# Kernel optimization log

Hardware: AMD Instinct MI355X
Metric: run time of the kernel (lower is better)

Reference implementation:

```python
import jax, jax.numpy as jnp
from jax import lax
import numpy as np

# --- constants from Vessel_Enhance_Block defaults ---
MIN_MAX = (0.0, 500.0)
ALPHA, BETA, GAMMA = 0.5, 1.0, 5.0          # frangi_param[0:3]
SIGMAS = tuple(np.arange(1.0, 2.5, 0.3).tolist())  # [1.0,1.3,1.6,1.9,2.2]
FRANGI_TH = 0.2
TH_LO, TH_HI = 0.1, 0.5                     # th_param
MIN_SIZE = 200


def _gauss_kernel1d(sigma, order):
    """scipy.ndimage-style Gaussian derivative kernel (truncate=4)."""
    radius = int(4.0 * sigma + 0.5)
    x = np.arange(-radius, radius + 1)
    phi = np.exp(-0.5 * x ** 2 / sigma ** 2)
    phi /= phi.sum()
    if order == 0:
        return phi
    exps = np.arange(order + 1)
    q = np.zeros(order + 1); q[0] = 1.0
    D = np.diag(exps[1:], 1)
    P = np.diag(np.full(order, -1.0 / sigma ** 2), -1)
    for _ in range(order):
        q = (D + P) @ q
    return (x[:, None].astype(float) ** exps @ q) * phi


def _corr1d(x, k, axis):
    """scipy gaussian_filter1d == correlate with k[::-1] == convolve with k.
    lax.conv is a correlation, so pass k reversed. mode='reflect' (symmetric)."""
    x = jnp.moveaxis(x, axis, -1)
    shp = x.shape
    r = (k.shape[0] - 1) // 2
    xp = jnp.pad(x.reshape(-1, 1, shp[-1]), ((0, 0), (0, 0), (r, r)), mode='symmetric')
    kern = jnp.asarray(k[::-1].copy(), x.dtype).reshape(1, 1, -1)
    y = lax.conv_general_dilated(xp, kern, (1,), 'VALID')
    return jnp.moveaxis(y.reshape(shp), -1, axis)


def _frangi(img):
    """2D Frangi vesselness, black_ridges=False, img: [B,H,W]."""
    img = -img  # black_ridges=False -> negate image
    out = jnp.zeros_like(img)
    for sigma in SIGMAS:
        k0 = _gauss_kernel1d(sigma, 0)
        k1 = _gauss_kernel1d(sigma, 1)
        k2 = _gauss_kernel1d(sigma, 2)
        s2 = jnp.asarray(sigma ** 2, img.dtype)  # scale normalization
        Hrr = _corr1d(_corr1d(img, k2, 1), k0, 2) * s2
        Hrc = _corr1d(_corr1d(img, k1, 1), k1, 2) * s2
        Hcc = _corr1d(_corr1d(img, k0, 1), k2, 2) * s2
        mid = 0.5 * (Hrr + Hcc)
        disc = jnp.sqrt(jnp.square(0.5 * (Hrr - Hcc)) + jnp.square(Hrc))
        e_hi, e_lo = mid + disc, mid - disc
        small = jnp.abs(e_hi) <= jnp.abs(e_lo)  # sort eigenvalues by magnitude
        lam1 = jnp.where(small, e_hi, e_lo)     # |lam1| <= |lam2|
        lam2 = jnp.where(small, e_lo, e_hi)
        lam2c = jnp.maximum(lam2, 1e-10)
        r_b2 = jnp.square(lam1 / lam2c)                       # blobness^2
        s_sq = jnp.square(lam1) + jnp.square(lam2)            # structuredness^2
        vals = jnp.exp(-r_b2 / (2.0 * BETA ** 2)) * (1.0 - jnp.exp(-s_sq / (2.0 * GAMMA ** 2)))
        out = jnp.maximum(out, vals)
    return out


def _remove_small(mask, min_size):
    """remove_small_objects(connectivity=2): drop 8-connected components < min_size."""
    H, W = mask.shape
    BIG = H * W
    idx = jnp.arange(BIG, dtype=jnp.int32).reshape(H, W)
    lab0 = jnp.where(mask, idx, BIG)

    def nmin(lab):  # min over 8-neighborhood, restricted to mask
        p = jnp.pad(lab, 1, constant_values=BIG)
        m = lab
        for di in (0, 1, 2):
            for dj in (0, 1, 2):
                if di == 1 and dj == 1:
                    continue
                m = jnp.minimum(m, lax.dynamic_slice(p, (di, dj), (H, W)))
        return jnp.where(mask, m, BIG)

    def jump(lab):  # pointer jumping: lab <- lab[lab]
        flat = lab.reshape(-1)
        ext = jnp.concatenate([flat, jnp.array([BIG], flat.dtype)])
        return ext[flat].reshape(H, W)

    def body(st):
        lab, _ = st
        return jump(jump(nmin(lab))), lab

    def cond(st):
        lab, prev = st
        return jnp.any(lab != prev)

    lab, _ = lax.while_loop(cond, body, (nmin(lab0), lab0))
    sizes = jnp.zeros(BIG + 1, jnp.int32).at[lab.reshape(-1)].add(mask.reshape(-1).astype(jnp.int32))
    return (sizes[lab] >= min_size) & mask


def setup_inputs() -> dict:
    key = jax.random.key(0)
    image = jax.random.uniform(key, (16, 1, 512, 512), dtype=jnp.float32)
    return {"image": image}


def reference(image):
    x = image[:, 0]                                   # [B,H,W]
    th_mask = (x >= TH_LO) & (x <= TH_HI)             # get_th
    scaled = x * (MIN_MAX[1] - MIN_MAX[0]) + MIN_MAX[0]
    fr = _frangi(scaled)
    fmask = th_mask & (fr >= FRANGI_TH)               # th & frangi masks
    out = jax.vmap(lambda m: _remove_small(m, MIN_SIZE))(fmask)
    return out[:, None]                               # [B,1,H,W] bool
```

## Files before the change

kernel.cpp:

```cpp
#include <hip/hip_runtime.h>
#include <math.h>
#include <string.h>

#define IMG_H   512
#define IMG_W   512
#define NPIX    (IMG_H*IMG_W)
#define NIMG    16
#define NSIG    5
#define MIN_SZ  200
#define SSTR    60
#define SROWS   52
#define TSTR    68
#define KVL     20
#define KHL     24
#define NBLK    65536

typedef float f4 __attribute__((ext_vector_type(4)));
typedef float f2 __attribute__((ext_vector_type(2)));

struct KTab {
  float kv[NSIG][3][KVL];
  float kh[NSIG][3][KHL];
  float s2[NSIG];
};

__device__ __forceinline__ void pkfma(f2 &acc, f2 x, f2 w) {
  asm("v_pk_fma_f32 %0, %1, %2, %0"
      : "+v"(acc) : "v"(x), "v"(w));
}

template<int SIG, int RAD, int MLO, int GH, int LP4, int L4P>
__device__ __forceinline__ void do_sigma(const float* __restrict__ sIn,
                                         float* __restrict__ t0,
                                         float* __restrict__ t1,
                                         float* __restrict__ t2,
                                         const KTab& kt, int tid, float* fr)
{
  if (tid < 32*GH) {
    int r0 = tid & 31;
    int h  = tid >> 5;
    int a  = (r0 + 9 - RAD)*SSTR + 4*(MLO + 2*h);
    f2 A0l={0,0},A0h={0,0},A1l={0,0},A1h={0,0},A2l={0,0},A2h={0,0};
    f2 B0l={0,0},B0h={0,0},B1l={0,0},B1h={0,0},B2l={0,0},B2h={0,0};
#pragma unroll 1
    for (int jj = 0; jj < LP4/4; ++jj) {
      f4 w0 = *(const f4*)&kt.kv[SIG][0][4*jj];
      f4 w1 = *(const f4*)&kt.kv[SIG][1][4*jj];
      f4 w2 = *(const f4*)&kt.kv[SIG][2][4*jj];
#pragma unroll
      for (int u = 0; u < 4; ++u) {
        f4 xA = *(const f4*)(sIn + a);
        f4 xB = *(const f4*)(sIn + a + 4);
        a += SSTR;
        f2 xAl = __builtin_shufflevector(xA, xA, 0, 1);
        f2 xAh = __builtin_shufflevector(xA, xA, 2, 3);
        f2 xBl = __builtin_shufflevector(xB, xB, 0, 1);
        f2 xBh = __builtin_shufflevector(xB, xB, 2, 3);
        f2 wv0 = {w0[u], w0[u]};
        f2 wv1 = {w1[u], w1[u]};
        f2 wv2 = {w2[u], w2[u]};
        pkfma(A0l, xAl, wv0); pkfma(A0h, xAh, wv0);
        pkfma(A1l, xAl, wv1); pkfma(A1h, xAh, wv1);
        pkfma(A2l, xAl, wv2); pkfma(A2h, xAh, wv2);
        pkfma(B0l, xBl, wv0); pkfma(B0h, xBh, wv0);
        pkfma(B1l, xBl, wv1); pkfma(B1h, xBh, wv1);
        pkfma(B2l, xBl, wv2); pkfma(B2h, xBh, wv2);
      }
    }
    int tb = r0*TSTR + 4*(MLO + 2*h);
    *(f4*)(t0 + tb)     = __builtin_shufflevector(A0l, A0h, 0,1,2,3);
    *(f4*)(t1 + tb)     = __builtin_shufflevector(A1l, A1h, 0,1,2,3);
    *(f4*)(t2 + tb)     = __builtin_shufflevector(A2l, A2h, 0,1,2,3);
    *(f4*)(t0 + tb + 4) = __builtin_shufflevector(B0l, B0h, 0,1,2,3);
    *(f4*)(t1 + tb + 4) = __builtin_shufflevector(B1l, B1h, 0,1,2,3);
    *(f4*)(t2 + tb + 4) = __builtin_shufflevector(B2l, B2h, 0,1,2,3);
  }
  __syncthreads();

  {
    int r  = tid >> 3;
    int c0 = (tid & 7) * 4;
    int wa = r*TSTR + 4*MLO + c0;
    f4 P0 = *(const f4*)(t0 + wa);
    f4 P1 = *(const f4*)(t1 + wa);
    f4 P2 = *(const f4*)(t2 + wa);
    f4 Q0 = *(const f4*)(t0 + wa + 4);
    f4 Q1 = *(const f4*)(t1 + wa + 4);
    f4 Q2 = *(const f4*)(t2 + wa + 4);
    wa += 8;
    f4 hrr={0,0,0,0}, hrc={0,0,0,0}, hcc={0,0,0,0};
#pragma unroll 1
    for (int aa = 0; aa < L4P/8; ++aa) {
      {
        f4 w0 = *(const f4*)&kt.kh[SIG][0][8*aa];
        f4 w1 = *(const f4*)&kt.kh[SIG][1][8*aa];
        f4 w2 = *(const f4*)&kt.kh[SIG][2][8*aa];
#pragma unroll
        for (int b = 0; b < 4; ++b)
#pragma unroll
          for (int k = 0; k < 4; ++k) {
            int e = b + k;
            float x2 = (e < 4) ? P2[e] : Q2[e-4];
            float x1 = (e < 4) ? P1[e] : Q1[e-4];
            float x0 = (e < 4) ? P0[e] : Q0[e-4];
            hrr[k] += x2 * w0[b];
            hrc[k] += x1 * w1[b];
            hcc[k] += x0 * w2[b];
          }
        P0 = *(const f4*)(t0 + wa);
        P1 = *(const f4*)(t1 + wa);
        P2 = *(const f4*)(t2 + wa);
      }
      {
        f4 w0 = *(const f4*)&kt.kh[SIG][0][8*aa+4];
        f4 w1 = *(const f4*)&kt.kh[SIG][1][8*aa+4];
        f4 w2 = *(const f4*)&kt.kh[SIG][2][8*aa+4];
#pragma unroll
        for (int b = 0; b < 4; ++b)
#pragma unroll
          for (int k = 0; k < 4; ++k) {
            int e = b + k;
            float x2 = (e < 4) ? Q2[e] : P2[e-4];
            float x1 = (e < 4) ? Q1[e] : P1[e-4];
            float x0 = (e < 4) ? Q0[e] : P0[e-4];
            hrr[k] += x2 * w0[b];
            hrc[k] += x1 * w1[b];
            hcc[k] += x0 * w2[b];
          }
        Q0 = *(const f4*)(t0 + wa + 4);
        Q1 = *(const f4*)(t1 + wa + 4);
        Q2 = *(const f4*)(t2 + wa + 4);
      }
      wa += 8;
    }
    float s2v = kt.s2[SIG];
#pragma unroll
    for (int k = 0; k < 4; ++k) {
      float Hrr = hrr[k]*s2v, Hrc = hrc[k]*s2v, Hcc = hcc[k]*s2v;
      float mid  = 0.5f*(Hrr + Hcc);
      float dif  = 0.5f*(Hrr - Hcc);
      float disc = sqrtf(dif*dif + Hrc*Hrc);
      float ehi  = mid + disc;
      float elo  = mid - disc;
      bool  sm   = fabsf(ehi) <= fabsf(elo);
      float lam1 = sm ? ehi : elo;
      float lam2 = sm ? elo : ehi;
      float lam2c = fmaxf(lam2, 1e-10f);
      float q    = lam1 / lam2c;
      float rb2  = q*q;
      float ssq  = lam1*lam1 + lam2*lam2;
      float v    = expf((-rb2)/2.0f) * (1.0f - expf((-ssq)/50.0f));
      fr[k] = fmaxf(fr[k], v);
    }
  }
  __syncthreads();
}

__global__ __launch_bounds__(256)
void frangi_label_kernel(const float* __restrict__ img,
                         int* __restrict__ labels,
                         int* __restrict__ parent,
                         int* __restrict__ bsizes,
                         KTab kt)
{
  __shared__ float sIn[SROWS*SSTR];
  __shared__ float t0[32*TSTR];
  __shared__ float t1[32*TSTR];
  __shared__ float t2[32*TSTR];

  const int tid    = threadIdx.x;
  const int imgIdx = blockIdx.y;
  const int tIdx   = blockIdx.x;
  const int tr0    = (tIdx >> 4) * 32;
  const int tc0    = (tIdx & 15) * 32;
  const float* __restrict__ im = img + (size_t)imgIdx * NPIX;

  for (int idx = tid; idx < SROWS*64; idx += 256) {
    int r  = idx >> 6;
    int cs = idx & 63;
    if (cs < SSTR) {
      float v = 0.0f;
      if (r < 50 && cs >= 3 && cs < 53) {
        int gr = tr0 + r - 9;
        int gc = tc0 + cs - 12;
        gr = (gr < 0) ? (-1 - gr) : ((gr >= IMG_H) ? (2*IMG_H - 1 - gr) : gr);
        gc = (gc < 0) ? (-1 - gc) : ((gc >= IMG_W) ? (2*IMG_W - 1 - gc) : gc);
        v = -(im[gr*IMG_W + gc] * 500.0f);
      }
      sIn[r*SSTR + cs] = v;
    }
  }
  __syncthreads();

  float fr[4] = {0.0f, 0.0f, 0.0f, 0.0f};
  do_sigma<0,  4,  2,  6, 12, 16>(sIn, t0, t1, t2, kt, tid, fr);
  do_sigma<1,  5,  1,  6, 12, 16>(sIn, t0, t1, t2, kt, tid, fr);
  do_sigma<2,  6,  1,  6, 16, 16>(sIn, t0, t1, t2, kt, tid, fr);
  do_sigma<3,  8,  1,  7, 20, 24>(sIn, t0, t1, t2, kt, tid, fr);
  do_sigma<4,  9,  0,  7, 20, 24>(sIn, t0, t1, t2, kt, tid, fr);

  const int r  = tid >> 3;
  const int c0 = (tid & 7) * 4;
  const int gr = tr0 + r;
  const size_t imgBase = (size_t)imgIdx * NPIX;
#pragma unroll
  for (int k = 0; k < 4; ++k) {
    int p = gr*IMG_W + tc0 + c0 + k;
    float x = im[p];
    bool m = (x >= 0.1f) && (x <= 0.5f) && (fr[k] >= 0.2f);
    labels[imgBase + p] = m ? p : -1;
  }
  {
    int blk = (tr0/2 + (tid >> 4))*256 + (tc0/2 + (tid & 15));
    int o   = (imgIdx << 16) + blk;
    parent[o] = blk;
    bsizes[o] = 0;
  }
}

__device__ __forceinline__ int ldA(const int* p) {
  return __hip_atomic_load(p, __ATOMIC_RELAXED, __HIP_MEMORY_SCOPE_AGENT);
}
__device__ __forceinline__ int rootOf(const int* L, int x) {
  int pa = ldA(&L[x]);
  while (pa != x) { int g = ldA(&L[pa]); x = pa; pa = g; }
  return x;
}
__device__ __forceinline__ void unite(int* P, int a, int b) {
  while (true) {
    a = rootOf(P, a);
    b = rootOf(P, b);
    if (a == b) return;
    int hi = a > b ? a : b;
    int lo = a ^ b ^ hi;
    int old = atomicCAS(&P[hi], hi, lo);
    if (old == hi) return;
    a = old; b = lo;
  }
}

__global__ __launch_bounds__(256)
void merge_kernel(const int* __restrict__ labels, int* __restrict__ parent)
{
  int gid = blockIdx.x*256 + threadIdx.x;
  int img = gid >> 16;
  int blk = gid & (NBLK - 1);
  int BR = blk >> 8, BC = blk & 255;
  const int* L = labels + ((size_t)img << 18);
  int p = BR*1024 + BC*2;
  int2 t = *(const int2*)(L + p);
  int2 bm = *(const int2*)(L + p + 512);
  bool f00 = t.x >= 0, f01 = t.y >= 0, f10 = bm.x >= 0, f11 = bm.y >= 0;
  if (!(f00 | f01 | f10 | f11)) return;
  int* P = parent + (img << 16);
  if (BC > 0 && (f00 | f10) && (L[p-1] >= 0 || L[p+511] >= 0))
    unite(P, blk, blk-1);
  if (BR > 0) {
    int2 n = *(const int2*)(L + p - 512);
    if ((f00 | f01) && (n.x >= 0 || n.y >= 0)) unite(P, blk, blk-256);
    if (BC > 0   && f00 && L[p-513] >= 0)      unite(P, blk, blk-257);
    if (BC < 255 && f01 && L[p-510] >= 0)      unite(P, blk, blk-255);
  }
}

__global__ __launch_bounds__(256)
void compress_count_kernel(const int* __restrict__ labels,
                           int* __restrict__ parent, int* __restrict__ bsizes)
{
  int gid = blockIdx.x*256 + threadIdx.x;
  int img = gid >> 16;
  int blk = gid & (NBLK - 1);
  int BR = blk >> 8, BC = blk & 255;
  const int* L = labels + ((size_t)img << 18);
  int p = BR*1024 + BC*2;
  int2 t = *(const int2*)(L + p);
  int2 bm = *(const int2*)(L + p + 512);
  int cnt = (t.x >= 0) + (t.y >= 0) + (bm.x >= 0) + (bm.y >= 0);
  int* P = parent + (img << 16);
  int rt = -1;
  if (cnt) {
    rt = rootOf(P, blk);
    __hip_atomic_store(&P[blk], rt, __ATOMIC_RELAXED, __HIP_MEMORY_SCOPE_AGENT);
  }
  int lane = threadIdx.x & 63;
  int val  = cnt;
  int prt  = __shfl_up(rt, 1);
  int fseg = (lane == 0 || prt != rt) ? 1 : 0;
#pragma unroll
  for (int d = 1; d < 64; d <<= 1) {
    int v2  = __shfl_up(val, d);
    int fg2 = __shfl_up(fseg, d);
    if (lane >= d && !fseg) { val += v2; fseg |= fg2; }
  }
  int nrt = __shfl_down(rt, 1);
  bool tail = (lane == 63) || (nrt != rt);
  if (tail && rt >= 0)
    atomicAdd(&bsizes[(img << 16) + rt], val);
}

__global__ __launch_bounds__(256)
void output_kernel(const int* __restrict__ labels, const int* __restrict__ parent,
                   const int* __restrict__ bsizes, float* __restrict__ out)
{
  int qid = blockIdx.x*256 + threadIdx.x;
  int img = qid >> 16;
  int p0  = (qid & 65535) << 2;
  const int* L = labels + ((size_t)img << 18);
  int4 l4 = *(const int4*)(L + p0);
  int r = p0 >> 9, c = p0 & 511;
  int blk0 = (r >> 1)*256 + (c >> 1);
  const int* P = parent + (img << 16);
  const int* S = bsizes + (img << 16);
  int2 pp = *(const int2*)(P + blk0);
  float4 o;
  o.x = (l4.x >= 0 && S[pp.x] >= MIN_SZ) ? 1.0f : 0.0f;
  o.y = (l4.y >= 0 && S[pp.x] >= MIN_SZ) ? 1.0f : 0.0f;
  o.z = (l4.z >= 0 && S[pp.y] >= MIN_SZ) ? 1.0f : 0.0f;
  o.w = (l4.w >= 0 && S[pp.y] >= MIN_SZ) ? 1.0f : 0.0f;
  *(float4*)(out + ((size_t)qid << 2)) = o;
}

static void gauss1d(double sigma, int order, int rad, float* out)
{
  int L = 2*rad + 1;
  double phi[24];
  double s = 0.0;
  for (int i = 0; i < L; ++i) {
    double x = (double)(i - rad);
    phi[i] = exp(-0.5*x*x/(sigma*sigma));
    s += phi[i];
  }
  for (int i = 0; i < L; ++i) phi[i] /= s;
  if (order == 0) {
    for (int i = 0; i < L; ++i) out[i] = (float)phi[i];
    return;
  }
  double q[3] = {1.0, 0.0, 0.0};
  for (int it = 0; it < order; ++it) {
    double nq[3] = {0.0, 0.0, 0.0};
    for (int i = 0; i <= order; ++i) {
      double v = 0.0;
      if (i+1 <= order) v += (double)(i+1) * q[i+1];
      if (i-1 >= 0)     v += (-1.0/(sigma*sigma)) * q[i-1];
      nq[i] = v;
    }
    q[0] = nq[0]; q[1] = nq[1]; q[2] = nq[2];
  }
  for (int i = 0; i < L; ++i) {
    double x = (double)(i - rad);
    double poly = q[0];
    double xp = x;
    for (int e = 1; e <= order; ++e) { poly += xp*q[e]; xp *= x; }
    out[i] = (float)(poly*phi[i]);
  }
}

extern "C" void kernel_launch(void* const* d_in, const int* in_sizes, int n_in,
                              void* d_out, int out_size, void* d_ws, size_t ws_size,
                              hipStream_t stream)
{
  (void)in_sizes; (void)n_in; (void)out_size; (void)ws_size;
  const float* img = (const float*)d_in[0];
  float* out = (float*)d_out;
  int* labels = (int*)d_ws;
  int* parent = labels + (size_t)NIMG * NPIX;
  int* bsizes = parent + (size_t)NIMG * NBLK;

  KTab kt;
  memset(&kt, 0, sizeof(kt));
  for (int s = 0; s < NSIG; ++s) {
    double sigma = 1.0 + 0.3 * (double)s;
    int rad = (int)(4.0 * sigma + 0.5);
    int L   = 2*rad + 1;
    int dlt = (12 - rad) & 3;
    kt.s2[s] = (float)(sigma * sigma);
    float k[3][24];
    for (int o = 0; o < 3; ++o) gauss1d(sigma, o, rad, k[o]);
    for (int o = 0; o < 3; ++o) {
      for (int j = 0; j < L; ++j)
        kt.kv[s][o][j] = k[o][L-1-j];
      for (int jp = 0; jp < KHL; ++jp)
        kt.kh[s][o][jp] = (jp >= dlt && jp - dlt < L) ? k[o][L-1-(jp-dlt)] : 0.0f;
    }
  }

  dim3 gridF(NPIX / (32*32), NIMG);
  frangi_label_kernel<<<gridF, 256, 0, stream>>>(img, labels, parent, bsizes, kt);

  int bblocks = (NIMG * NBLK) / 256;
  merge_kernel         <<<bblocks, 256, 0, stream>>>(labels, parent);
  compress_count_kernel<<<bblocks, 256, 0, stream>>>(labels, parent, bsizes);
  output_kernel        <<<bblocks, 256, 0, stream>>>(labels, parent, bsizes, out);
}
```

Before: 214.5 us.

## Restructure vertical Gaussian pass to compute two output rows per thread with exact taps

The vertical convolution pass now has each thread produce two adjacent output rows for one 4-column group. Each loaded input row is reused for both rows through a one-step-delayed weight, and the loop runs over exactly the kernel length instead of a padded multiple of four. The packed-FMA inline asm is replaced with plain f4 vector FMAs. LDS strides are shrunk and merged into one buffer that is zeroed up front, and a redundant prefetch after the last horizontal iteration is guarded. This cuts LDS reads and padded FMAs in the vertical pass, at the cost of an extra zero-fill pass and reliance on the compiler to emit packed math.

```diff
diff --git a/kernel.cpp b/kernel.cpp
--- a/kernel.cpp
+++ b/kernel.cpp
@@ -8,15 +8,15 @@
 #define NIMG    16
 #define NSIG    5
 #define MIN_SZ  200
-#define SSTR    60
-#define SROWS   52
-#define TSTR    68
+#define SSTR    56
+#define SROWS   50
+#define TSTR    56
+#define TSZ     (32*TSTR)
 #define KVL     20
 #define KHL     24
 #define NBLK    65536
 
 typedef float f4 __attribute__((ext_vector_type(4)));
-typedef float f2 __attribute__((ext_vector_type(2)));
 
 struct KTab {
   float kv[NSIG][3][KVL];
@@ -24,56 +24,36 @@
   float s2[NSIG];
 };
 
-__device__ __forceinline__ void pkfma(f2 &acc, f2 x, f2 w) {
-  asm("v_pk_fma_f32 %0, %1, %2, %0"
-      : "+v"(acc) : "v"(x), "v"(w));
-}
-
-template<int SIG, int RAD, int MLO, int GH, int LP4, int L4P>
+template<int SIG, int RAD, int MLO, int G, int L4P>
 __device__ __forceinline__ void do_sigma(const float* __restrict__ sIn,
                                          float* __restrict__ t0,
                                          float* __restrict__ t1,
                                          float* __restrict__ t2,
                                          const KTab& kt, int tid, float* fr)
 {
-  if (tid < 32*GH) {
-    int r0 = tid & 31;
-    int h  = tid >> 5;
-    int a  = (r0 + 9 - RAD)*SSTR + 4*(MLO + 2*h);
-    f2 A0l={0,0},A0h={0,0},A1l={0,0},A1h={0,0},A2l={0,0},A2h={0,0};
-    f2 B0l={0,0},B0h={0,0},B1l={0,0},B1h={0,0},B2l={0,0},B2h={0,0};
+  constexpr int L = 2*RAD + 1;
+
+  if (tid < 16*G) {
+    int g  = tid % G;
+    int rp = tid / G;
+    int r0 = rp*2;
+    int a  = (r0 + 9 - RAD)*SSTR + 4*(MLO + g);
+    f4 a00={0,0,0,0}, a01={0,0,0,0}, a02={0,0,0,0};
+    f4 a10={0,0,0,0}, a11={0,0,0,0}, a12={0,0,0,0};
+    float w0c=0.0f, w1c=0.0f, w2c=0.0f;
 #pragma unroll 1
-    for (int jj = 0; jj < LP4/4; ++jj) {
-      f4 w0 = *(const f4*)&kt.kv[SIG][0][4*jj];
-      f4 w1 = *(const f4*)&kt.kv[SIG][1][4*jj];
-      f4 w2 = *(const f4*)&kt.kv[SIG][2][4*jj];
-#pragma unroll
-      for (int u = 0; u < 4; ++u) {
-        f4 xA = *(const f4*)(sIn + a);
-        f4 xB = *(const f4*)(sIn + a + 4);
-        a += SSTR;
-        f2 xAl = __builtin_shufflevector(xA, xA, 0, 1);
-        f2 xAh = __builtin_shufflevector(xA, xA, 2, 3);
-        f2 xBl = __builtin_shufflevector(xB, xB, 0, 1);
-        f2 xBh = __builtin_shufflevector(xB, xB, 2, 3);
-        f2 wv0 = {w0[u], w0[u]};
-        f2 wv1 = {w1[u], w1[u]};
-        f2 wv2 = {w2[u], w2[u]};
-        pkfma(A0l, xAl, wv0); pkfma(A0h, xAh, wv0);
-        pkfma(A1l, xAl, wv1); pkfma(A1h, xAh, wv1);
-        pkfma(A2l, xAl, wv2); pkfma(A2h, xAh, wv2);
-        pkfma(B0l, xBl, wv0); pkfma(B0h, xBh, wv0);
-        pkfma(B1l, xBl, wv1); pkfma(B1h, xBh, wv1);
-        pkfma(B2l, xBl, wv2); pkfma(B2h, xBh, wv2);
-      }
-    }
-    int tb = r0*TSTR + 4*(MLO + 2*h);
-    *(f4*)(t0 + tb)     = __builtin_shufflevector(A0l, A0h, 0,1,2,3);
-    *(f4*)(t1 + tb)     = __builtin_shufflevector(A1l, A1h, 0,1,2,3);
-    *(f4*)(t2 + tb)     = __builtin_shufflevector(A2l, A2h, 0,1,2,3);
-    *(f4*)(t0 + tb + 4) = __builtin_shufflevector(B0l, B0h, 0,1,2,3);
-    *(f4*)(t1 + tb + 4) = __builtin_shufflevector(B1l, B1h, 0,1,2,3);
-    *(f4*)(t2 + tb + 4) = __builtin_shufflevector(B2l, B2h, 0,1,2,3);
+    for (int m = 0; m <= L; ++m) {
+      float w0p=w0c, w1p=w1c, w2p=w2c;
+      w0c = kt.kv[SIG][0][m];
+      w1c = kt.kv[SIG][1][m];
+      w2c = kt.kv[SIG][2][m];
+      f4 x = *(const f4*)(sIn + a); a += SSTR;
+      a00 += x*w0c; a01 += x*w1c; a02 += x*w2c;
+      a10 += x*w0p; a11 += x*w1p; a12 += x*w2p;
+    }
+    int tb = r0*TSTR + 4*(MLO + g);
+    *(f4*)(t0+tb)      = a00; *(f4*)(t1+tb)      = a01; *(f4*)(t2+tb)      = a02;
+    *(f4*)(t0+tb+TSTR) = a10; *(f4*)(t1+tb+TSTR) = a11; *(f4*)(t2+tb+TSTR) = a12;
   }
   __syncthreads();
 
@@ -127,9 +107,11 @@
             hrc[k] += x1 * w1[b];
             hcc[k] += x0 * w2[b];
           }
-        Q0 = *(const f4*)(t0 + wa + 4);
-        Q1 = *(const f4*)(t1 + wa + 4);
-        Q2 = *(const f4*)(t2 + wa + 4);
+        if (aa + 1 < L4P/8) {
+          Q0 = *(const f4*)(t0 + wa + 4);
+          Q1 = *(const f4*)(t1 + wa + 4);
+          Q2 = *(const f4*)(t2 + wa + 4);
+        }
       }
       wa += 8;
     }
@@ -163,10 +145,11 @@
                          int* __restrict__ bsizes,
                          KTab kt)
 {
-  __shared__ float sIn[SROWS*SSTR];
-  __shared__ float t0[32*TSTR];
-  __shared__ float t1[32*TSTR];
-  __shared__ float t2[32*TSTR];
+  __shared__ float lds[3*TSZ + SROWS*SSTR];
+  float* t0  = lds;
+  float* t1  = lds + TSZ;
+  float* t2  = lds + 2*TSZ;
+  float* sIn = lds + 3*TSZ;
 
   const int tid    = threadIdx.x;
   const int imgIdx = blockIdx.y;
@@ -175,12 +158,13 @@
   const int tc0    = (tIdx & 15) * 32;
   const float* __restrict__ im = img + (size_t)imgIdx * NPIX;
 
+  for (int i = tid; i < 3*TSZ; i += 256) lds[i] = 0.0f;
   for (int idx = tid; idx < SROWS*64; idx += 256) {
     int r  = idx >> 6;
     int cs = idx & 63;
     if (cs < SSTR) {
       float v = 0.0f;
-      if (r < 50 && cs >= 3 && cs < 53) {
+      if (cs >= 3 && cs < 53) {
         int gr = tr0 + r - 9;
         int gc = tc0 + cs - 12;
         gr = (gr < 0) ? (-1 - gr) : ((gr >= IMG_H) ? (2*IMG_H - 1 - gr) : gr);
@@ -193,11 +177,11 @@
   __syncthreads();
 
   float fr[4] = {0.0f, 0.0f, 0.0f, 0.0f};
-  do_sigma<0,  4,  2,  6, 12, 16>(sIn, t0, t1, t2, kt, tid, fr);
-  do_sigma<1,  5,  1,  6, 12, 16>(sIn, t0, t1, t2, kt, tid, fr);
-  do_sigma<2,  6,  1,  6, 16, 16>(sIn, t0, t1, t2, kt, tid, fr);
-  do_sigma<3,  8,  1,  7, 20, 24>(sIn, t0, t1, t2, kt, tid, fr);
-  do_sigma<4,  9,  0,  7, 20, 24>(sIn, t0, t1, t2, kt, tid, fr);
+  do_sigma<0,  4,  2, 12, 16>(sIn, t0, t1, t2, kt, tid, fr);
+  do_sigma<1,  5,  1, 12, 16>(sIn, t0, t1, t2, kt, tid, fr);
+  do_sigma<2,  6,  1, 12, 16>(sIn, t0, t1, t2, kt, tid, fr);
+  do_sigma<3,  8,  1, 13, 24>(sIn, t0, t1, t2, kt, tid, fr);
+  do_sigma<4,  9,  0, 14, 24>(sIn, t0, t1, t2, kt, tid, fr);
 
   const int r  = tid >> 3;
   const int c0 = (tid & 7) * 4;
```

New measurement: 219.9 us. 1.03x slower.
